# Kernel tuning notes

Measured on AMD Instinct MI355X. Metric: run time of the kernel, lower is better.

Reference implementation:

```python
import math
import jax, jax.numpy as jnp
import numpy as np

B, T, C, HS = 4, 4096, 2048, 128

def setup_inputs() -> dict:
    key = jax.random.key(0)
    k1, k2, k3, k4 = jax.random.split(key, 4)
    x = jax.random.normal(k1, (B, T, C), dtype=jnp.float32)
    # torch Linear init ~ U(-1/sqrt(in), 1/sqrt(in)); normal*0.02 is fine for a numeric baseline
    Wq = jax.random.normal(k2, (C, HS), dtype=jnp.float32) * 0.02
    Wk = jax.random.normal(k3, (C, HS), dtype=jnp.float32) * 0.02
    Wv = jax.random.normal(k4, (C, HS), dtype=jnp.float32) * 0.02
    return {"x": x, "Wq": Wq, "Wk": Wk, "Wv": Wv}

def reference(x, Wq, Wk, Wv):
    # Single-head causal self-attention (dropout in eval mode = identity).
    q = x @ Wq          # [B,T,HS]
    k = x @ Wk          # [B,T,HS]
    v = x @ Wv          # [B,T,HS]
    scale = 1.0 / math.sqrt(HS)
    att = jnp.einsum('bqd,bkd->bqk', q, k) * scale          # [B,T,T]
    causal = jnp.tril(jnp.ones((T, T), dtype=bool))          # [T,T]
    att = jnp.where(causal[None, :, :], att, -jnp.inf)
    att = jax.nn.softmax(att, axis=-1)
    y = jnp.einsum('bqk,bkd->bqd', att, v)                   # [B,T,HS]
    return y
```

## Files before the change

### kernel.cpp

```cpp
#include <hip/hip_runtime.h>
#include <hip/hip_bf16.h>


#define B_  4
#define T_  4096
#define C_  2048
#define HS_ 128

typedef unsigned short u16;
typedef __attribute__((ext_vector_type(8))) short short8;
typedef __attribute__((ext_vector_type(4))) float floatx4;

static __device__ __forceinline__ u16 f2bf(float x) {
  union { float f; unsigned u; } c; c.f = x;
  unsigned r = 0x7fffu + ((c.u >> 16) & 1u);
  return (u16)((c.u + r) >> 16);
}

#define BAR_LDS()                                                  \
  do {                                                             \
    __asm__ volatile("s_waitcnt lgkmcnt(0)" ::: "memory");         \
    __builtin_amdgcn_s_barrier();                                  \
  } while (0)

__global__ __launch_bounds__(256) void wtrans3_kernel(
    const float* __restrict__ Wq, const float* __restrict__ Wk,
    const float* __restrict__ Wv, u16* __restrict__ dst) {
  __shared__ u16 tile[32][33];
  int z = blockIdx.z;
  const float* src = (z == 0) ? Wq : (z == 1) ? Wk : Wv;
  u16* d = dst + (size_t)z * HS_ * C_;
  int c0 = blockIdx.x * 32, r0 = blockIdx.y * 32;
  int tx = threadIdx.x, ty = threadIdx.y;
#pragma unroll
  for (int i = 0; i < 4; ++i)
    tile[ty + 8 * i][tx] = f2bf(src[(size_t)(r0 + ty + 8 * i) * HS_ + (c0 + tx)]);
  __syncthreads();
#pragma unroll
  for (int i = 0; i < 4; ++i)
    d[(size_t)(c0 + ty + 8 * i) * C_ + (r0 + tx)] = tile[tx][ty + 8 * i];
}

#define GBM 64
#define GBK 64
#define LPAD 72

__global__ __launch_bounds__(256) void qkv_gemm_kernel(
    const float* __restrict__ X, const u16* __restrict__ WT3,
    u16* __restrict__ qkv, u16* __restrict__ vT) {
  __shared__ u16 smem[GBM * LPAD + HS_ * LPAD];
  u16 (*Xs)[LPAD] = (u16(*)[LPAD])smem;
  u16 (*Ws)[LPAD] = (u16(*)[LPAD])(smem + GBM * LPAD);

  int z = blockIdx.y;
  const u16* Wt = WT3 + (size_t)z * HS_ * C_;
  int t = threadIdx.x;
  int wv = t >> 6, lane = t & 63;
  int l15 = lane & 15, hi = lane >> 4;
  int wm = (wv & 1) * 32, wn = (wv >> 1) * 64;
  size_t mbase = (size_t)blockIdx.x * GBM;

  int xm = t >> 3, xc = t & 7;

  const float* xrow0 = &X[(mbase + xm) * C_];
  const float* xrow1 = &X[(mbase + 32 + xm) * C_];
  const u16* wrow0 = &Wt[(size_t)(xm) * C_];
  const u16* wrow1 = &Wt[(size_t)(32 + xm) * C_];
  const u16* wrow2 = &Wt[(size_t)(64 + xm) * C_];
  const u16* wrow3 = &Wt[(size_t)(96 + xm) * C_];

  floatx4 acc[2][4];
#pragma unroll
  for (int i = 0; i < 2; ++i)
#pragma unroll
    for (int j = 0; j < 4; ++j) acc[i][j] = (floatx4){0.f, 0.f, 0.f, 0.f};

  floatx4 xreg[2][2];
  short8 wreg[4];
  {
    int koff = xc * 8;
    xreg[0][0] = *(const floatx4*)&xrow0[koff];
    xreg[0][1] = *(const floatx4*)&xrow0[koff + 4];
    xreg[1][0] = *(const floatx4*)&xrow1[koff];
    xreg[1][1] = *(const floatx4*)&xrow1[koff + 4];
    wreg[0] = *(const short8*)&wrow0[koff];
    wreg[1] = *(const short8*)&wrow1[koff];
    wreg[2] = *(const short8*)&wrow2[koff];
    wreg[3] = *(const short8*)&wrow3[koff];
  }

  for (int kt = 0; kt < C_ / GBK; ++kt) {
#pragma unroll
    for (int i = 0; i < 2; ++i) {
      short8 v;
#pragma unroll
      for (int j = 0; j < 4; ++j) {
        v[j] = (short)f2bf(xreg[i][0][j]);
        v[4 + j] = (short)f2bf(xreg[i][1][j]);
      }
      *(short8*)&Xs[i * 32 + xm][xc * 8] = v;
    }
    *(short8*)&Ws[xm][xc * 8] = wreg[0];
    *(short8*)&Ws[32 + xm][xc * 8] = wreg[1];
    *(short8*)&Ws[64 + xm][xc * 8] = wreg[2];
    *(short8*)&Ws[96 + xm][xc * 8] = wreg[3];
    BAR_LDS();

    if (kt + 1 < C_ / GBK) {
      int koff = (kt + 1) * GBK + xc * 8;
      xreg[0][0] = *(const floatx4*)&xrow0[koff];
      xreg[0][1] = *(const floatx4*)&xrow0[koff + 4];
      xreg[1][0] = *(const floatx4*)&xrow1[koff];
      xreg[1][1] = *(const floatx4*)&xrow1[koff + 4];
      wreg[0] = *(const short8*)&wrow0[koff];
      wreg[1] = *(const short8*)&wrow1[koff];
      wreg[2] = *(const short8*)&wrow2[koff];
      wreg[3] = *(const short8*)&wrow3[koff];
    }

#pragma unroll
    for (int ks = 0; ks < 2; ++ks) {
      short8 af[2], bf[4];
#pragma unroll
      for (int mt = 0; mt < 2; ++mt)
        af[mt] = *(const short8*)&Xs[wm + mt * 16 + l15][ks * 32 + hi * 8];
#pragma unroll
      for (int nt = 0; nt < 4; ++nt)
        bf[nt] = *(const short8*)&Ws[wn + nt * 16 + l15][ks * 32 + hi * 8];
#pragma unroll
      for (int mt = 0; mt < 2; ++mt)
#pragma unroll
        for (int nt = 0; nt < 4; ++nt)
          acc[mt][nt] = __builtin_amdgcn_mfma_f32_16x16x32_bf16(
              af[mt], bf[nt], acc[mt][nt], 0, 0, 0);
    }
    BAR_LDS();
  }

  if (z != 2) {
    u16* outp = qkv + (size_t)z * ((size_t)B_ * T_ * HS_);
#pragma unroll
    for (int mt = 0; mt < 2; ++mt)
#pragma unroll
      for (int nt = 0; nt < 4; ++nt)
#pragma unroll
        for (int r = 0; r < 4; ++r) {
          size_t row = mbase + wm + mt * 16 + hi * 4 + r;
          int col = wn + nt * 16 + l15;
          outp[row * HS_ + col] = f2bf(acc[mt][nt][r]);
        }
  } else {
    u16 (*Tb)[LPAD] = (u16(*)[LPAD])smem;
#pragma unroll
    for (int mt = 0; mt < 2; ++mt)
#pragma unroll
      for (int nt = 0; nt < 4; ++nt)
#pragma unroll
        for (int r = 0; r < 4; ++r)
          Tb[wn + nt * 16 + l15][wm + mt * 16 + hi * 4 + r] = f2bf(acc[mt][nt][r]);
    __syncthreads();
    int b = (int)(mbase >> 12);
    int trow0 = (int)(mbase & (T_ - 1));
    u16* vb = vT + (size_t)b * HS_ * T_;
#pragma unroll
    for (int i = 0; i < 4; ++i) {
      int id = i * 256 + t;
      int c = id >> 3, ch = id & 7;
      short8 v = *(const short8*)&Tb[c][ch * 8];
      *(short8*)&vb[(size_t)c * T_ + trow0 + ch * 8] = v;
    }
  }
}

#define BQ 64
#define BKV 64
#define CHUNK 16

template <bool WRITE_PARTIAL>
static __device__ __forceinline__ void flash_body(
    const u16* __restrict__ q, const u16* __restrict__ k,
    const u16* __restrict__ vT, float* __restrict__ outO,
    float* __restrict__ Mp, float* __restrict__ Lp,
    int b, int qb, int kb0, int kb1, int slot) {
  __shared__ u16 Ks[BKV][136];
  __shared__ u16 Vs[144][72];
  __shared__ u16 Ps[BQ][72];
  int t = threadIdx.x;
  int wv = t >> 6, lane = t & 63, l15 = lane & 15, hi = lane >> 4;

  const float sc = 0.08838834764831845f * 1.4426950408889634f;

  short8 qf[4];
  {
    const u16* qrow = q + (size_t)(b * T_ + qb * BQ + wv * 16 + l15) * HS_;
#pragma unroll
    for (int ks = 0; ks < 4; ++ks)
      qf[ks] = *(const short8*)(qrow + ks * 32 + hi * 8);
  }

  {
    int r = 128 + (t >> 4), c0 = (t & 15) * 4;
    const u16 one = 0x3F80;
    Vs[r][c0] = one; Vs[r][c0 + 1] = one;
    Vs[r][c0 + 2] = one; Vs[r][c0 + 3] = one;
  }

  floatx4 of[9];
#pragma unroll
  for (int dt = 0; dt < 9; ++dt) of[dt] = (floatx4){0.f, 0.f, 0.f, 0.f};
  float m_run[4];
#pragma unroll
  for (int r = 0; r < 4; ++r) m_run[r] = -__builtin_inff();

  const u16* kbase = k + (size_t)b * T_ * HS_;
  const u16* vbase = vT + (size_t)b * HS_ * T_;

  short8 kreg[4], vreg[4];
#pragma unroll
  for (int i = 0; i < 4; ++i) {
    int id = i * 256 + t;
    int n = id >> 4, ck = id & 15;
    kreg[i] = *(const short8*)&kbase[(size_t)(kb0 * BKV + n) * HS_ + ck * 8];
    int d = id >> 3, cv = id & 7;
    vreg[i] = *(const short8*)&vbase[(size_t)d * T_ + kb0 * BKV + cv * 8];
  }

  for (int kb = kb0; kb <= kb1; ++kb) {
#pragma unroll
    for (int i = 0; i < 4; ++i) {
      int id = i * 256 + t;
      int n = id >> 4, ck = id & 15;
      *(short8*)&Ks[n][ck * 8] = kreg[i];
      int d = id >> 3, cv = id & 7;
      *(short8*)&Vs[d][cv * 8] = vreg[i];
    }
    BAR_LDS();

    if (kb < kb1) {
#pragma unroll
      for (int i = 0; i < 4; ++i) {
        int id = i * 256 + t;
        int n = id >> 4, ck = id & 15;
        kreg[i] = *(const short8*)&kbase[(size_t)((kb + 1) * BKV + n) * HS_ + ck * 8];
        int d = id >> 3, cv = id & 7;
        vreg[i] = *(const short8*)&vbase[(size_t)d * T_ + (kb + 1) * BKV + cv * 8];
      }
    }

    floatx4 sf[4];
#pragma unroll
    for (int nt = 0; nt < 4; ++nt) {
      floatx4 s = (floatx4){0.f, 0.f, 0.f, 0.f};
#pragma unroll
      for (int ks = 0; ks < 4; ++ks) {
        short8 bfrag = *(const short8*)&Ks[nt * 16 + l15][ks * 32 + hi * 8];
        s = __builtin_amdgcn_mfma_f32_16x16x32_bf16(qf[ks], bfrag, s, 0, 0, 0);
      }
      sf[nt] = s;
    }

    float sv[4][4];
    if (kb == qb) {
#pragma unroll
      for (int nt = 0; nt < 4; ++nt) {
        int col = nt * 16 + l15;
#pragma unroll
        for (int r = 0; r < 4; ++r) {
          int row = wv * 16 + hi * 4 + r;
          sv[nt][r] = (col <= row) ? sf[nt][r] * sc : -__builtin_inff();
        }
      }
    } else {
#pragma unroll
      for (int nt = 0; nt < 4; ++nt)
#pragma unroll
        for (int r = 0; r < 4; ++r) sv[nt][r] = sf[nt][r] * sc;
    }

    float mt4[4];
#pragma unroll
    for (int r = 0; r < 4; ++r)
      mt4[r] = fmaxf(fmaxf(sv[0][r], sv[1][r]), fmaxf(sv[2][r], sv[3][r]));
#pragma unroll
    for (int off = 1; off < 16; off <<= 1)
#pragma unroll
      for (int r = 0; r < 4; ++r)
        mt4[r] = fmaxf(mt4[r], __shfl_xor(mt4[r], off));

    bool need = false;
#pragma unroll
    for (int r = 0; r < 4; ++r) need = need || (mt4[r] > m_run[r] + 8.f);
    if (__any(need)) {
      float alpha[4];
#pragma unroll
      for (int r = 0; r < 4; ++r) {
        float mn = fmaxf(m_run[r], mt4[r]);
        alpha[r] = exp2f(m_run[r] - mn);
        m_run[r] = mn;
      }
#pragma unroll
      for (int dt = 0; dt < 9; ++dt)
#pragma unroll
        for (int r = 0; r < 4; ++r) of[dt][r] *= alpha[r];
    }

    float pv[4][4];
#pragma unroll
    for (int nt = 0; nt < 4; ++nt)
#pragma unroll
      for (int r = 0; r < 4; ++r) pv[nt][r] = exp2f(sv[nt][r] - m_run[r]);

#pragma unroll
    for (int nt = 0; nt < 4; ++nt)
#pragma unroll
      for (int r = 0; r < 4; ++r)
        Ps[wv * 16 + hi * 4 + r][nt * 16 + l15] = f2bf(pv[nt][r]);
    __asm__ volatile("s_waitcnt lgkmcnt(0)" ::: "memory");

#pragma unroll
    for (int ks2 = 0; ks2 < 2; ++ks2) {
      short8 af = *(const short8*)&Ps[wv * 16 + l15][ks2 * 32 + hi * 8];
#pragma unroll
      for (int dt = 0; dt < 9; ++dt) {
        short8 bfrag = *(const short8*)&Vs[dt * 16 + l15][ks2 * 32 + hi * 8];
        of[dt] = __builtin_amdgcn_mfma_f32_16x16x32_bf16(af, bfrag, of[dt], 0, 0, 0);
      }
    }
    BAR_LDS();
  }

  if (WRITE_PARTIAL) {
    float* Op = outO + (size_t)slot * (BQ * HS_);
#pragma unroll
    for (int dt = 0; dt < 8; ++dt)
#pragma unroll
      for (int r = 0; r < 4; ++r) {
        int row = wv * 16 + hi * 4 + r;
        Op[row * HS_ + dt * 16 + l15] = of[dt][r];
      }
    if (l15 == 0) {
#pragma unroll
      for (int r = 0; r < 4; ++r) {
        int row = wv * 16 + hi * 4 + r;
        Mp[slot * BQ + row] = m_run[r];
        Lp[slot * BQ + row] = of[8][r];
      }
    }
  } else {
    float rl[4];
#pragma unroll
    for (int r = 0; r < 4; ++r) rl[r] = 1.0f / of[8][r];
#pragma unroll
    for (int dt = 0; dt < 8; ++dt)
#pragma unroll
      for (int r = 0; r < 4; ++r) {
        size_t row = (size_t)(b * T_ + qb * BQ + wv * 16 + hi * 4 + r);
        outO[row * HS_ + dt * 16 + l15] = of[dt][r] * rl[r];
      }
  }
}

__global__ __launch_bounds__(256, 3) void flash_partial_kernel(
    const u16* __restrict__ q, const u16* __restrict__ k,
    const u16* __restrict__ vT, float* __restrict__ Opart,
    float* __restrict__ Mpart, float* __restrict__ Lpart) {
  int qb = blockIdx.x, c = blockIdx.y, b = blockIdx.z;
  int kb0 = c * CHUNK;
  if (kb0 > qb) return;
  int kb1 = min(qb, kb0 + CHUNK - 1);
  int slot = (b * (T_ / BQ) + qb) * 4 + c;
  flash_body<true>(q, k, vT, Opart, Mpart, Lpart, b, qb, kb0, kb1, slot);
}

__global__ __launch_bounds__(256, 3) void flash_attn_kernel(
    const u16* __restrict__ q, const u16* __restrict__ k,
    const u16* __restrict__ vT, float* __restrict__ out) {
  int qb = blockIdx.x, b = blockIdx.y;
  flash_body<false>(q, k, vT, out, nullptr, nullptr, b, qb, 0, qb, 0);
}

__global__ __launch_bounds__(256) void flash_merge_kernel(
    const float* __restrict__ Opart, const float* __restrict__ Mpart,
    const float* __restrict__ Lpart, float* __restrict__ out) {
  __shared__ float w[4][BQ];
  __shared__ float invL[BQ];
  int qb = blockIdx.x, b = blockIdx.y;
  int t = threadIdx.x;
  int nch = qb / CHUNK + 1;
  int slot0 = (b * (T_ / BQ) + qb) * 4;

  if (t < BQ) {
    float mv[4], mmax = -__builtin_inff();
    for (int c = 0; c < nch; ++c) {
      mv[c] = Mpart[(slot0 + c) * BQ + t];
      mmax = fmaxf(mmax, mv[c]);
    }
    float L = 0.f;
    for (int c = 0; c < nch; ++c) {
      float wc = exp2f(mv[c] - mmax);
      w[c][t] = wc;
      L += wc * Lpart[(slot0 + c) * BQ + t];
    }
    invL[t] = 1.0f / L;
  }
  __syncthreads();

  size_t obase = ((size_t)(b * T_) + (size_t)qb * BQ) * HS_;
#pragma unroll
  for (int j = 0; j < 32; ++j) {
    int e = j * 256 + t;
    int row = e >> 7;
    float acc = 0.f;
    for (int c = 0; c < nch; ++c)
      acc += w[c][row] * Opart[(size_t)(slot0 + c) * (BQ * HS_) + e];
    out[obase + e] = acc * invL[row];
  }
}

extern "C" void kernel_launch(void* const* d_in, const int* in_sizes, int n_in,
                              void* d_out, int out_size, void* d_ws, size_t ws_size,
                              hipStream_t stream) {
  const float* x  = (const float*)d_in[0];
  const float* Wq = (const float*)d_in[1];
  const float* Wk = (const float*)d_in[2];
  const float* Wv = (const float*)d_in[3];
  float* out = (float*)d_out;

  u16* ws = (u16*)d_ws;
  const size_t wtsz  = (size_t)HS_ * C_;
  const size_t qkvsz = (size_t)B_ * T_ * HS_;
  u16* WT = ws;
  u16* qv = WT + 3 * wtsz;
  u16* kv = qv + qkvsz;
  u16* vT = kv + qkvsz;
  const size_t base_bytes = (3 * wtsz + 3 * qkvsz) * sizeof(u16);

  const int NSLOT = B_ * (T_ / BQ) * 4;
  float* Opart = (float*)((char*)d_ws + base_bytes);
  float* Mpart = Opart + (size_t)NSLOT * BQ * HS_;
  float* Lpart = Mpart + (size_t)NSLOT * BQ;
  const size_t split_bytes =
      base_bytes + ((size_t)NSLOT * BQ * HS_ + 2 * (size_t)NSLOT * BQ) * sizeof(float);

  dim3 tb(32, 8);
  wtrans3_kernel<<<dim3(HS_ / 32, C_ / 32, 3), tb, 0, stream>>>(Wq, Wk, Wv, WT);

  qkv_gemm_kernel<<<dim3((B_ * T_) / GBM, 3), 256, 0, stream>>>(x, WT, qv, vT);

  if (ws_size >= split_bytes) {
    flash_partial_kernel<<<dim3(T_ / BQ, 4, B_), 256, 0, stream>>>(
        qv, kv, vT, Opart, Mpart, Lpart);
    flash_merge_kernel<<<dim3(T_ / BQ, B_), 256, 0, stream>>>(
        Opart, Mpart, Lpart, out);
  } else {
    flash_attn_kernel<<<dim3(T_ / BQ, B_), 256, 0, stream>>>(qv, kv, vT, out);
  }
}
```

Before: 308.8 us.

## Store split-KV partials in bf16, finalize single-chunk blocks directly, reverse block order

Partial attention outputs are now stored as bf16 instead of fp32, which halves the write and read traffic between the partial and merge kernels. The merge kernel reads them with vectorized short8 loads and writes with float4 stores. Query blocks that need only one chunk write the normalized output directly and skip the merge. Query blocks are scheduled in reverse so the longest work starts first. Rounding unnormalized partials to bf16 adds some error to the result.

Result: slower. 319.3 us (+3.4%).

```diff
diff --git a/kernel.cpp b/kernel.cpp
--- a/kernel.cpp
+++ b/kernel.cpp
@@ -15,6 +15,10 @@
   union { float f; unsigned u; } c; c.f = x;
   unsigned r = 0x7fffu + ((c.u >> 16) & 1u);
   return (u16)((c.u + r) >> 16);
+}
+static __device__ __forceinline__ float bf2f(u16 x) {
+  union { unsigned u; float f; } c; c.u = ((unsigned)x) << 16;
+  return c.f;
 }
 
 #define BAR_LDS()                                                  \
@@ -179,8 +183,8 @@
 template <bool WRITE_PARTIAL>
 static __device__ __forceinline__ void flash_body(
     const u16* __restrict__ q, const u16* __restrict__ k,
-    const u16* __restrict__ vT, float* __restrict__ outO,
-    float* __restrict__ Mp, float* __restrict__ Lp,
+    const u16* __restrict__ vT, float* __restrict__ outF,
+    u16* __restrict__ OpartP, float* __restrict__ Mp, float* __restrict__ Lp,
     int b, int qb, int kb0, int kb1, int slot) {
   __shared__ u16 Ks[BKV][136];
   __shared__ u16 Vs[144][72];
@@ -330,13 +334,13 @@
   }
 
   if (WRITE_PARTIAL) {
-    float* Op = outO + (size_t)slot * (BQ * HS_);
+    u16* Op = OpartP + (size_t)slot * (BQ * HS_);
 #pragma unroll
     for (int dt = 0; dt < 8; ++dt)
 #pragma unroll
       for (int r = 0; r < 4; ++r) {
         int row = wv * 16 + hi * 4 + r;
-        Op[row * HS_ + dt * 16 + l15] = of[dt][r];
+        Op[row * HS_ + dt * 16 + l15] = f2bf(of[dt][r]);
       }
     if (l15 == 0) {
 #pragma unroll
@@ -355,36 +359,44 @@
 #pragma unroll
       for (int r = 0; r < 4; ++r) {
         size_t row = (size_t)(b * T_ + qb * BQ + wv * 16 + hi * 4 + r);
-        outO[row * HS_ + dt * 16 + l15] = of[dt][r] * rl[r];
+        outF[row * HS_ + dt * 16 + l15] = of[dt][r] * rl[r];
       }
   }
 }
 
 __global__ __launch_bounds__(256, 3) void flash_partial_kernel(
     const u16* __restrict__ q, const u16* __restrict__ k,
-    const u16* __restrict__ vT, float* __restrict__ Opart,
-    float* __restrict__ Mpart, float* __restrict__ Lpart) {
-  int qb = blockIdx.x, c = blockIdx.y, b = blockIdx.z;
+    const u16* __restrict__ vT, u16* __restrict__ Opart,
+    float* __restrict__ Mpart, float* __restrict__ Lpart,
+    float* __restrict__ out) {
+  int qb = (T_ / BQ - 1) - blockIdx.x, c = blockIdx.y, b = blockIdx.z;
   int kb0 = c * CHUNK;
   if (kb0 > qb) return;
   int kb1 = min(qb, kb0 + CHUNK - 1);
-  int slot = (b * (T_ / BQ) + qb) * 4 + c;
-  flash_body<true>(q, k, vT, Opart, Mpart, Lpart, b, qb, kb0, kb1, slot);
+  if (qb < CHUNK) {
+    flash_body<false>(q, k, vT, out, nullptr, nullptr, nullptr,
+                      b, qb, kb0, kb1, 0);
+  } else {
+    int slot = (b * (T_ / BQ) + qb) * 4 + c;
+    flash_body<true>(q, k, vT, nullptr, Opart, Mpart, Lpart,
+                     b, qb, kb0, kb1, slot);
+  }
 }
 
 __global__ __launch_bounds__(256, 3) void flash_attn_kernel(
     const u16* __restrict__ q, const u16* __restrict__ k,
     const u16* __restrict__ vT, float* __restrict__ out) {
   int qb = blockIdx.x, b = blockIdx.y;
-  flash_body<false>(q, k, vT, out, nullptr, nullptr, b, qb, 0, qb, 0);
+  flash_body<false>(q, k, vT, out, nullptr, nullptr, nullptr, b, qb, 0, qb, 0);
 }
 
 __global__ __launch_bounds__(256) void flash_merge_kernel(
-    const float* __restrict__ Opart, const float* __restrict__ Mpart,
+    const u16* __restrict__ Opart, const float* __restrict__ Mpart,
     const float* __restrict__ Lpart, float* __restrict__ out) {
   __shared__ float w[4][BQ];
   __shared__ float invL[BQ];
   int qb = blockIdx.x, b = blockIdx.y;
+  if (qb < CHUNK) return;
   int t = threadIdx.x;
   int nch = qb / CHUNK + 1;
   int slot0 = (b * (T_ / BQ) + qb) * 4;
@@ -407,13 +419,24 @@
 
   size_t obase = ((size_t)(b * T_) + (size_t)qb * BQ) * HS_;
 #pragma unroll
-  for (int j = 0; j < 32; ++j) {
-    int e = j * 256 + t;
-    int row = e >> 7;
-    float acc = 0.f;
-    for (int c = 0; c < nch; ++c)
-      acc += w[c][row] * Opart[(size_t)(slot0 + c) * (BQ * HS_) + e];
-    out[obase + e] = acc * invL[row];
+  for (int j = 0; j < 4; ++j) {
+    int e8 = (j * 256 + t) * 8;
+    int row = e8 >> 7;
+    float accf[8];
+#pragma unroll
+    for (int u = 0; u < 8; ++u) accf[u] = 0.f;
+    for (int c = 0; c < nch; ++c) {
+      short8 v = *(const short8*)&Opart[(size_t)(slot0 + c) * (BQ * HS_) + e8];
+      float wc = w[c][row];
+#pragma unroll
+      for (int u = 0; u < 8; ++u) accf[u] += wc * bf2f((u16)v[u]);
+    }
+    float rl = invL[row];
+    floatx4 o0, o1;
+#pragma unroll
+    for (int u = 0; u < 4; ++u) { o0[u] = accf[u] * rl; o1[u] = accf[4 + u] * rl; }
+    *(floatx4*)&out[obase + e8] = o0;
+    *(floatx4*)&out[obase + e8 + 4] = o1;
   }
 }
 
@@ -436,11 +459,12 @@
   const size_t base_bytes = (3 * wtsz + 3 * qkvsz) * sizeof(u16);
 
   const int NSLOT = B_ * (T_ / BQ) * 4;
-  float* Opart = (float*)((char*)d_ws + base_bytes);
-  float* Mpart = Opart + (size_t)NSLOT * BQ * HS_;
+  u16* Opart = (u16*)((char*)d_ws + base_bytes);
+  float* Mpart = (float*)(Opart + (size_t)NSLOT * BQ * HS_);
   float* Lpart = Mpart + (size_t)NSLOT * BQ;
   const size_t split_bytes =
-      base_bytes + ((size_t)NSLOT * BQ * HS_ + 2 * (size_t)NSLOT * BQ) * sizeof(float);
+      base_bytes + (size_t)NSLOT * BQ * HS_ * sizeof(u16) +
+      2 * (size_t)NSLOT * BQ * sizeof(float);
 
   dim3 tb(32, 8);
   wtrans3_kernel<<<dim3(HS_ / 32, C_ / 32, 3), tb, 0, stream>>>(Wq, Wk, Wv, WT);
@@ -449,7 +473,7 @@
 
   if (ws_size >= split_bytes) {
     flash_partial_kernel<<<dim3(T_ / BQ, 4, B_), 256, 0, stream>>>(
-        qv, kv, vT, Opart, Mpart, Lpart);
+        qv, kv, vT, Opart, Mpart, Lpart, out);
     flash_merge_kernel<<<dim3(T_ / BQ, B_), 256, 0, stream>>>(
         Opart, Mpart, Lpart, out);
   } else {
```
